# Performance work log

Measured on AMD Instinct MI355X. Metric: run time of the kernel, lower is better.

The kernel has to match this reference:

```python
import jax, jax.numpy as jnp
import numpy as np

B, N, D4 = 32768, 20, 64  # embed_dim = 4 * D4 = 256
BIG = 1e10


def setup_inputs() -> dict:
    key = jax.random.key(0)
    ks = jax.random.split(key, 10)
    points = jax.random.normal(ks[0], (B, N, 3), dtype=jnp.float32)
    mask = (jax.random.uniform(ks[1], (B, N)) < 0.85).astype(jnp.float32)
    s = 0.1
    return {
        "points": points,
        "mask": mask,
        "W_rel": jax.random.normal(ks[2], (3, D4), jnp.float32) * s,
        "b_rel": jax.random.normal(ks[3], (D4,), jnp.float32) * s,
        "W_dist": jax.random.normal(ks[4], (1, D4), jnp.float32) * s,
        "b_dist": jax.random.normal(ks[5], (D4,), jnp.float32) * s,
        "emb_count": jax.random.normal(ks[6], (50, D4), jnp.float32) * s,
        "W_den": jax.random.normal(ks[7], (1, D4), jnp.float32) * s,
        "b_den": jax.random.normal(ks[8], (D4,), jnp.float32) * s,
    }


def _local_density(points, mask):
    # Batched replacement of the per-sample cdist+topk Python loop.
    b, n, _ = points.shape
    diff = points[:, :, None, :] - points[:, None, :, :]        # [B,N,N,3]
    d2 = jnp.sum(diff * diff, axis=-1)                          # [B,N,N]
    eye = jnp.eye(n, dtype=bool)
    pair_valid = (mask[:, :, None] > 0) & (mask[:, None, :] > 0) & ~eye
    d = jnp.where(pair_valid, jnp.sqrt(jnp.maximum(d2, 1e-12)), BIG)
    nearest = -jax.lax.top_k(-d, 3)[0]                          # 3 smallest dists, ascending
    nv = jnp.sum(mask, axis=1).astype(jnp.int32)                # [B] valid counts
    k = jnp.clip(jnp.minimum(3, nv - 1), 1, None)               # k = min(3, n_valid-1)
    w = (jnp.arange(3)[None, :] < k[:, None]).astype(points.dtype)  # [B,3]
    dens = jnp.sum(nearest * w[:, None, :], axis=-1) / k[:, None].astype(points.dtype)
    valid_row = (mask > 0) & (nv[:, None] > 1)                  # zero for invalid / n_valid<=1
    return jnp.where(valid_row, dens, 0.0)[..., None]           # [B,N,1]


def reference(points, mask, W_rel, b_rel, W_dist, b_dist, emb_count, W_den, b_den):
    b, n, _ = points.shape
    n_valid = jnp.clip(jnp.sum(mask, axis=1, keepdims=True), 1, None)    # [B,1]
    centroid = jnp.sum(points * mask[..., None], axis=1, keepdims=True) / n_valid[..., None]
    rel = points - centroid                                              # [B,N,3]
    rel_f = rel @ W_rel + b_rel                                          # [B,N,D4]
    cdist_ = jnp.linalg.norm(rel, axis=-1, keepdims=True)                # [B,N,1]
    dist_f = cdist_ @ W_dist + b_dist                                    # [B,N,D4]
    idx = n_valid[:, 0].astype(jnp.int32)                                # [B]
    count_f = jnp.broadcast_to(emb_count[idx][:, None, :], (b, n, emb_count.shape[1]))
    density = _local_density(points, mask)                               # [B,N,1]
    den_f = density @ W_den + b_den                                      # [B,N,D4]
    return jnp.concatenate([rel_f, dist_f, count_f, den_f], axis=-1)     # [B,N,4*D4]
```

## Files before the change

kernel.cpp:

```cpp
#include <hip/hip_runtime.h>
#include <math.h>

#define BIGD 1e10f
#define NPTS 20

__global__ __launch_bounds__(256) void spf_kernel(
    const float* __restrict__ points,
    const float* __restrict__ mask,
    const float* __restrict__ W_rel,
    const float* __restrict__ b_rel,
    const float* __restrict__ W_dist,
    const float* __restrict__ b_dist,
    const float* __restrict__ emb_count,
    const float* __restrict__ W_den,
    const float* __restrict__ b_den,
    float* __restrict__ out)
{
    const int b   = blockIdx.x;
    const int tid = threadIdx.x;

    __shared__ float sP[NPTS * 3];
    __shared__ float sM[NPTS];
    __shared__ float sDen[NPTS];
    __shared__ float sCd[NPTS];

    if (tid < NPTS * 3) sP[tid] = points[(size_t)b * (NPTS * 3) + tid];
    if (tid < NPTS)     sM[tid] = mask[(size_t)b * NPTS + tid];
    __syncthreads();

    float sm = 0.f, cx = 0.f, cy = 0.f, cz = 0.f;
#pragma unroll
    for (int i = 0; i < NPTS; ++i) {
        float m = sM[i];
        sm += m;
        cx = fmaf(m, sP[i * 3 + 0], cx);
        cy = fmaf(m, sP[i * 3 + 1], cy);
        cz = fmaf(m, sP[i * 3 + 2], cz);
    }
    const float nvf = fmaxf(sm, 1.0f);
    cx /= nvf; cy /= nvf; cz /= nvf;
    const int nv  = (int)(sm + 0.5f);
    const int idx = (int)(nvf + 0.5f);

    if (tid < NPTS) {
        const int i = tid;
        const float mi = sM[i];
        const float px = sP[i * 3 + 0], py = sP[i * 3 + 1], pz = sP[i * 3 + 2];
        float b0 = BIGD, b1 = BIGD, b2 = BIGD;
#pragma unroll
        for (int j = 0; j < NPTS; ++j) {
            const float dx = px - sP[j * 3 + 0];
            const float dy = py - sP[j * 3 + 1];
            const float dz = pz - sP[j * 3 + 2];
            const float d2 = dx * dx + dy * dy + dz * dz;
            float d = sqrtf(fmaxf(d2, 1e-12f));
            const bool valid = (j != i) && (mi > 0.f) && (sM[j] > 0.f);
            d = valid ? d : BIGD;
            if (d < b0)      { b2 = b1; b1 = b0; b0 = d; }
            else if (d < b1) { b2 = b1; b1 = d; }
            else if (d < b2) { b2 = d; }
        }
        int k = min(3, nv - 1);
        k = max(k, 1);
        float s = b0;
        if (k > 1) s += b1;
        if (k > 2) s += b2;
        const float dens = s / (float)k;
        sDen[i] = ((mi > 0.f) && (nv > 1)) ? dens : 0.f;

        const float rx = px - cx, ry = py - cy, rz = pz - cz;
        sCd[i] = sqrtf(rx * rx + ry * ry + rz * rz);
    }
    __syncthreads();

    const int g      = tid & 63;
    const int r0     = tid >> 6;
    const int region = g >> 4;
    const int cq     = g & 15;

    float4 w0 = {0, 0, 0, 0}, w1 = {0, 0, 0, 0}, w2 = {0, 0, 0, 0};
    float4 wd = {0, 0, 0, 0}, bb = {0, 0, 0, 0};
    if (region == 0) {
        w0 = ((const float4*)(W_rel +   0))[cq];
        w1 = ((const float4*)(W_rel +  64))[cq];
        w2 = ((const float4*)(W_rel + 128))[cq];
        bb = ((const float4*)b_rel)[cq];
    } else if (region == 1) {
        wd = ((const float4*)W_dist)[cq];
        bb = ((const float4*)b_dist)[cq];
    } else if (region == 2) {
        bb = ((const float4*)(emb_count + (size_t)idx * 64))[cq];
    } else {
        wd = ((const float4*)W_den)[cq];
        bb = ((const float4*)b_den)[cq];
    }
    const bool use_cd = (region == 1);

    float4* __restrict__ outv = (float4*)(out + (size_t)b * (NPTS * 256));
#pragma unroll
    for (int n = r0; n < NPTS; n += 4) {
        const float rx = sP[n * 3 + 0] - cx;
        const float ry = sP[n * 3 + 1] - cy;
        const float rz = sP[n * 3 + 2] - cz;
        const float sc = use_cd ? sCd[n] : sDen[n];
        float4 v;
        v.x = fmaf(rx, w0.x, fmaf(ry, w1.x, fmaf(rz, w2.x, fmaf(sc, wd.x, bb.x))));
        v.y = fmaf(rx, w0.y, fmaf(ry, w1.y, fmaf(rz, w2.y, fmaf(sc, wd.y, bb.y))));
        v.z = fmaf(rx, w0.z, fmaf(ry, w1.z, fmaf(rz, w2.z, fmaf(sc, wd.z, bb.z))));
        v.w = fmaf(rx, w0.w, fmaf(ry, w1.w, fmaf(rz, w2.w, fmaf(sc, wd.w, bb.w))));
        outv[n * 64 + g] = v;
    }
}

extern "C" void kernel_launch(void* const* d_in, const int* in_sizes, int n_in,
                              void* d_out, int out_size, void* d_ws, size_t ws_size,
                              hipStream_t stream) {
    const float* points    = (const float*)d_in[0];
    const float* mask      = (const float*)d_in[1];
    const float* W_rel     = (const float*)d_in[2];
    const float* b_rel     = (const float*)d_in[3];
    const float* W_dist    = (const float*)d_in[4];
    const float* b_dist    = (const float*)d_in[5];
    const float* emb_count = (const float*)d_in[6];
    const float* W_den     = (const float*)d_in[7];
    const float* b_den     = (const float*)d_in[8];
    float* out             = (float*)d_out;

    const int B = in_sizes[0] / (NPTS * 3);
    spf_kernel<<<B, 256, 0, stream>>>(points, mask, W_rel, b_rel, W_dist, b_dist,
                                      emb_count, W_den, b_den, out);
}
```

Baseline: 725.8 us.

## Map one wavefront per sample with vectorized loads and nontemporal output stores

Each 256-thread block now handles four samples, one per 64-lane wavefront, instead of one sample per block. The density computation now runs in 20 lanes of every wavefront rather than 20 threads of a whole block, so far fewer threads sit idle. Points and mask are loaded as float4 vectors. Output writes use nontemporal stores to avoid polluting the cache with the large write-only stream. The risk is that each wavefront now serially writes all 20 rows, and a bounds guard was added for partial blocks.

Measured after the change: 680.8 us. 1.07x faster.

```diff
diff --git a/kernel.cpp b/kernel.cpp
--- a/kernel.cpp
+++ b/kernel.cpp
@@ -3,6 +3,9 @@
 
 #define BIGD 1e10f
 #define NPTS 20
+#define BPB  4
+
+typedef float f4 __attribute__((ext_vector_type(4)));
 
 __global__ __launch_bounds__(256) void spf_kernel(
     const float* __restrict__ points,
@@ -14,47 +17,55 @@
     const float* __restrict__ emb_count,
     const float* __restrict__ W_den,
     const float* __restrict__ b_den,
-    float* __restrict__ out)
+    float* __restrict__ out,
+    int B)
 {
-    const int b   = blockIdx.x;
-    const int tid = threadIdx.x;
+    const int w    = threadIdx.x >> 6;
+    const int lane = threadIdx.x & 63;
+    const int b    = blockIdx.x * BPB + w;
+    const bool active = (b < B);
 
-    __shared__ float sP[NPTS * 3];
-    __shared__ float sM[NPTS];
-    __shared__ float sDen[NPTS];
-    __shared__ float sCd[NPTS];
+    __shared__ __align__(16) float sP[BPB][NPTS * 3];
+    __shared__ __align__(16) float sM[BPB][NPTS];
+    __shared__ float sDen[BPB][NPTS];
+    __shared__ float sCd[BPB][NPTS];
 
-    if (tid < NPTS * 3) sP[tid] = points[(size_t)b * (NPTS * 3) + tid];
-    if (tid < NPTS)     sM[tid] = mask[(size_t)b * NPTS + tid];
+    if (active) {
+        if (lane < 15) {
+            ((f4*)sP[w])[lane] = ((const f4*)points)[(size_t)b * 15 + lane];
+        } else if (lane < 20) {
+            ((f4*)sM[w])[lane - 15] = ((const f4*)mask)[(size_t)b * 5 + (lane - 15)];
+        }
+    }
     __syncthreads();
 
     float sm = 0.f, cx = 0.f, cy = 0.f, cz = 0.f;
 #pragma unroll
     for (int i = 0; i < NPTS; ++i) {
-        float m = sM[i];
+        const float m = sM[w][i];
         sm += m;
-        cx = fmaf(m, sP[i * 3 + 0], cx);
-        cy = fmaf(m, sP[i * 3 + 1], cy);
-        cz = fmaf(m, sP[i * 3 + 2], cz);
+        cx = fmaf(m, sP[w][i * 3 + 0], cx);
+        cy = fmaf(m, sP[w][i * 3 + 1], cy);
+        cz = fmaf(m, sP[w][i * 3 + 2], cz);
     }
     const float nvf = fmaxf(sm, 1.0f);
     cx /= nvf; cy /= nvf; cz /= nvf;
     const int nv  = (int)(sm + 0.5f);
     const int idx = (int)(nvf + 0.5f);
 
-    if (tid < NPTS) {
-        const int i = tid;
-        const float mi = sM[i];
-        const float px = sP[i * 3 + 0], py = sP[i * 3 + 1], pz = sP[i * 3 + 2];
+    if (active && lane < NPTS) {
+        const int i = lane;
+        const float mi = sM[w][i];
+        const float px = sP[w][i * 3 + 0], py = sP[w][i * 3 + 1], pz = sP[w][i * 3 + 2];
         float b0 = BIGD, b1 = BIGD, b2 = BIGD;
 #pragma unroll
         for (int j = 0; j < NPTS; ++j) {
-            const float dx = px - sP[j * 3 + 0];
-            const float dy = py - sP[j * 3 + 1];
-            const float dz = pz - sP[j * 3 + 2];
+            const float dx = px - sP[w][j * 3 + 0];
+            const float dy = py - sP[w][j * 3 + 1];
+            const float dz = pz - sP[w][j * 3 + 2];
             const float d2 = dx * dx + dy * dy + dz * dz;
             float d = sqrtf(fmaxf(d2, 1e-12f));
-            const bool valid = (j != i) && (mi > 0.f) && (sM[j] > 0.f);
+            const bool valid = (j != i) && (mi > 0.f) && (sM[w][j] > 0.f);
             d = valid ? d : BIGD;
             if (d < b0)      { b2 = b1; b1 = b0; b0 = d; }
             else if (d < b1) { b2 = b1; b1 = d; }
@@ -66,49 +77,50 @@
         if (k > 1) s += b1;
         if (k > 2) s += b2;
         const float dens = s / (float)k;
-        sDen[i] = ((mi > 0.f) && (nv > 1)) ? dens : 0.f;
+        sDen[w][i] = ((mi > 0.f) && (nv > 1)) ? dens : 0.f;
 
         const float rx = px - cx, ry = py - cy, rz = pz - cz;
-        sCd[i] = sqrtf(rx * rx + ry * ry + rz * rz);
+        sCd[w][i] = sqrtf(rx * rx + ry * ry + rz * rz);
     }
     __syncthreads();
 
-    const int g      = tid & 63;
-    const int r0     = tid >> 6;
+    const int g      = lane;
     const int region = g >> 4;
     const int cq     = g & 15;
 
-    float4 w0 = {0, 0, 0, 0}, w1 = {0, 0, 0, 0}, w2 = {0, 0, 0, 0};
-    float4 wd = {0, 0, 0, 0}, bb = {0, 0, 0, 0};
+    f4 w0 = {0,0,0,0}, w1 = {0,0,0,0}, w2 = {0,0,0,0};
+    f4 wd = {0,0,0,0}, bb = {0,0,0,0};
     if (region == 0) {
-        w0 = ((const float4*)(W_rel +   0))[cq];
-        w1 = ((const float4*)(W_rel +  64))[cq];
-        w2 = ((const float4*)(W_rel + 128))[cq];
-        bb = ((const float4*)b_rel)[cq];
+        w0 = ((const f4*)(W_rel +   0))[cq];
+        w1 = ((const f4*)(W_rel +  64))[cq];
+        w2 = ((const f4*)(W_rel + 128))[cq];
+        bb = ((const f4*)b_rel)[cq];
     } else if (region == 1) {
-        wd = ((const float4*)W_dist)[cq];
-        bb = ((const float4*)b_dist)[cq];
+        wd = ((const f4*)W_dist)[cq];
+        bb = ((const f4*)b_dist)[cq];
     } else if (region == 2) {
-        bb = ((const float4*)(emb_count + (size_t)idx * 64))[cq];
+        bb = ((const f4*)(emb_count + (size_t)idx * 64))[cq];
     } else {
-        wd = ((const float4*)W_den)[cq];
-        bb = ((const float4*)b_den)[cq];
+        wd = ((const f4*)W_den)[cq];
+        bb = ((const f4*)b_den)[cq];
     }
     const bool use_cd = (region == 1);
 
-    float4* __restrict__ outv = (float4*)(out + (size_t)b * (NPTS * 256));
+    if (active) {
+        f4* __restrict__ outv = (f4*)(out + (size_t)b * (NPTS * 256));
 #pragma unroll
-    for (int n = r0; n < NPTS; n += 4) {
-        const float rx = sP[n * 3 + 0] - cx;
-        const float ry = sP[n * 3 + 1] - cy;
-        const float rz = sP[n * 3 + 2] - cz;
-        const float sc = use_cd ? sCd[n] : sDen[n];
-        float4 v;
-        v.x = fmaf(rx, w0.x, fmaf(ry, w1.x, fmaf(rz, w2.x, fmaf(sc, wd.x, bb.x))));
-        v.y = fmaf(rx, w0.y, fmaf(ry, w1.y, fmaf(rz, w2.y, fmaf(sc, wd.y, bb.y))));
-        v.z = fmaf(rx, w0.z, fmaf(ry, w1.z, fmaf(rz, w2.z, fmaf(sc, wd.z, bb.z))));
-        v.w = fmaf(rx, w0.w, fmaf(ry, w1.w, fmaf(rz, w2.w, fmaf(sc, wd.w, bb.w))));
-        outv[n * 64 + g] = v;
+        for (int n = 0; n < NPTS; ++n) {
+            const float rx = sP[w][n * 3 + 0] - cx;
+            const float ry = sP[w][n * 3 + 1] - cy;
+            const float rz = sP[w][n * 3 + 2] - cz;
+            const float sc = use_cd ? sCd[w][n] : sDen[w][n];
+            f4 v;
+            v.x = fmaf(rx, w0.x, fmaf(ry, w1.x, fmaf(rz, w2.x, fmaf(sc, wd.x, bb.x))));
+            v.y = fmaf(rx, w0.y, fmaf(ry, w1.y, fmaf(rz, w2.y, fmaf(sc, wd.y, bb.y))));
+            v.z = fmaf(rx, w0.z, fmaf(ry, w1.z, fmaf(rz, w2.z, fmaf(sc, wd.z, bb.z))));
+            v.w = fmaf(rx, w0.w, fmaf(ry, w1.w, fmaf(rz, w2.w, fmaf(sc, wd.w, bb.w))));
+            __builtin_nontemporal_store(v, &outv[n * 64 + g]);
+        }
     }
 }
 
@@ -126,7 +138,8 @@
     const float* b_den     = (const float*)d_in[8];
     float* out             = (float*)d_out;
 
-    const int B = in_sizes[0] / (NPTS * 3);
-    spf_kernel<<<B, 256, 0, stream>>>(points, mask, W_rel, b_rel, W_dist, b_dist,
-                                      emb_count, W_den, b_den, out);
+    const int B    = in_sizes[0] / (NPTS * 3);
+    const int grid = (B + BPB - 1) / BPB;
+    spf_kernel<<<grid, 256, 0, stream>>>(points, mask, W_rel, b_rel, W_dist, b_dist,
+                                         emb_count, W_den, b_den, out, B);
 }
```
